# Kernel optimization log

Measured on AMD Instinct MI355X. Metric: run time of the kernel, lower is better.

## Reference

```python
import jax, jax.numpy as jnp
import numpy as np

D_MODEL = 1024
N_HEAD = 16
D_K = D_MODEL // N_HEAD


def setup_inputs() -> dict:
    key = jax.random.key(0)
    ks = jax.random.split(key, 11)
    B, S = 2, 2048
    std = 1.0 / np.sqrt(D_MODEL)
    inp = {
        "Q": jax.random.normal(ks[0], (B, S, D_MODEL), jnp.float32),
        "K": jax.random.normal(ks[1], (B, S, D_MODEL), jnp.float32),
        "V": jax.random.normal(ks[2], (B, S, D_MODEL), jnp.float32),
        "Wq": jax.random.normal(ks[3], (D_MODEL, D_MODEL), jnp.float32) * std,
        "bq": jnp.zeros((D_MODEL,), jnp.float32),
        "Wk": jax.random.normal(ks[4], (D_MODEL, D_MODEL), jnp.float32) * std,
        "bk": jnp.zeros((D_MODEL,), jnp.float32),
        "Wv": jax.random.normal(ks[5], (D_MODEL, D_MODEL), jnp.float32) * std,
        "bv": jnp.zeros((D_MODEL,), jnp.float32),
        "Wo": jax.random.normal(ks[6], (D_MODEL, D_MODEL), jnp.float32) * std,
        "bo": jnp.zeros((D_MODEL,), jnp.float32),
    }
    return inp


def _split_heads(x):
    # [B, S, D] -> [B, H, S, d_k]
    B, S, _ = x.shape
    return x.reshape(B, S, N_HEAD, D_K).transpose(0, 2, 1, 3)


def reference(Q, K, V, Wq, bq, Wk, bk, Wv, bv, Wo, bo):
    q = _split_heads(Q @ Wq.T + bq)   # [B,H,S,dk]
    k = _split_heads(K @ Wk.T + bk)
    v = _split_heads(V @ Wv.T + bv)
    scale = 1.0 / jnp.sqrt(jnp.float32(D_K))
    scores = jnp.einsum("bhqd,bhkd->bhqk", q, k) * scale
    attn = jax.nn.softmax(scores, axis=-1)
    ctx = jnp.einsum("bhqk,bhkd->bhqd", attn, v)  # [B,H,S,dk]
    B, H, S, dk = ctx.shape
    ctx = ctx.transpose(0, 2, 1, 3).reshape(B, S, H * dk)
    return ctx @ Wo.T + bo
```

## Files before the change

### kernel.cpp

```cpp
#include <hip/hip_runtime.h>
#include <hip/hip_bf16.h>
#include <cstdint>
#include <cstddef>
#include <cmath>

typedef __attribute__((ext_vector_type(8))) short short8;
typedef __attribute__((ext_vector_type(4))) short short4_t;
typedef __attribute__((ext_vector_type(4))) float f32x4;
typedef __attribute__((ext_vector_type(16))) float f32x16;

constexpr int B_ = 2, S_ = 2048, H_ = 16, DK_ = 64, DM_ = 1024;

__device__ inline unsigned short f2bf(float x) {
  union { float f; unsigned u; } c; c.f = x;
  unsigned r = c.u + 0x7FFF + ((c.u >> 16) & 1);
  return (unsigned short)(r >> 16);
}

__device__ inline float ex2(float x) {
#if __has_builtin(__builtin_amdgcn_exp2f)
  return __builtin_amdgcn_exp2f(x);
#else
  return exp2f(x);
#endif
}

__device__ inline unsigned pkbf(float lo, float hi) {
  unsigned u;
  asm("v_cvt_pk_bf16_f32 %0, %1, %2" : "=v"(u) : "v"(lo), "v"(hi));
  return u;
}

__device__ inline void plswap(unsigned& a, unsigned& b) {
#if __has_builtin(__builtin_amdgcn_permlane32_swap)
  auto r = __builtin_amdgcn_permlane32_swap(a, b, false, false);
  a = (unsigned)r[0];
  b = (unsigned)r[1];
#else
  unsigned sa = __shfl_xor(a, 32), sb = __shfl_xor(b, 32);
  unsigned lid = __builtin_amdgcn_mbcnt_hi(~0u, __builtin_amdgcn_mbcnt_lo(~0u, 0));
  bool hi = lid >= 32;
  unsigned na = hi ? sb : a;
  unsigned nb = hi ? b : sa;
  a = na; b = nb;
#endif
}

__device__ inline float red_half_sum(float x) {
  unsigned a = __float_as_uint(x), b = a;
  plswap(a, b);
  return __uint_as_float(a) + __uint_as_float(b);
}

__device__ inline f32x4 mfma16(short8 a, short8 b, f32x4 c) {
  return __builtin_amdgcn_mfma_f32_16x16x32_bf16(a, b, c, 0, 0, 0);
}
__device__ inline f32x16 mfma32(short8 a, short8 b, f32x16 c) {
  return __builtin_amdgcn_mfma_f32_32x32x16_bf16(a, b, c, 0, 0, 0);
}

__device__ inline void glds16(const unsigned short* g, unsigned short* l) {
  __builtin_amdgcn_global_load_lds(
      (const __attribute__((address_space(1))) unsigned int*)g,
      (__attribute__((address_space(3))) unsigned int*)l, 16, 0, 0);
}

__global__ __launch_bounds__(256) void cvt_all(
    const float* __restrict__ Q, const float* __restrict__ K,
    const float* __restrict__ V, const float* __restrict__ Wq,
    const float* __restrict__ Wk, const float* __restrict__ Wv,
    const float* __restrict__ Wo, unsigned short* __restrict__ Qb,
    unsigned short* __restrict__ Kb, unsigned short* __restrict__ Vb,
    unsigned short* __restrict__ Wqb, unsigned short* __restrict__ Wkb,
    unsigned short* __restrict__ Wvb, unsigned short* __restrict__ Wob) {
  int bid = blockIdx.x;
  const float* in; unsigned short* out; int off;
  if (bid < 4096)       { in = Q;  out = Qb;  off = bid; }
  else if (bid < 8192)  { in = K;  out = Kb;  off = bid - 4096; }
  else if (bid < 12288) { in = V;  out = Vb;  off = bid - 8192; }
  else if (bid < 13312) { in = Wq; out = Wqb; off = bid - 12288; }
  else if (bid < 14336) { in = Wk; out = Wkb; off = bid - 13312; }
  else if (bid < 15360) { in = Wv; out = Wvb; off = bid - 14336; }
  else                  { in = Wo; out = Wob; off = bid - 15360; }
  int i = off * 256 + threadIdx.x;
  float4 f = ((const float4*)in)[i];
  uint2 o;
  o.x = pkbf(f.x, f.y);
  o.y = pkbf(f.z, f.w);
  ((uint2*)out)[i] = o;
}

__device__ inline void store_out(float* p, float v) { *p = v; }
__device__ inline void store_out(unsigned short* p, float v) { *p = f2bf(v); }

template <typename OUT_T>
__device__ inline void gemm_k3_body(const unsigned short* __restrict__ A,
                                    const unsigned short* __restrict__ Bw,
                                    const float* __restrict__ bias,
                                    OUT_T* __restrict__ C, float cscale,
                                    int bm, int bn) {
  constexpr int Kd = 1024, Nd = 1024, NSTEP = Kd / 64;
  __shared__ unsigned short As[3][128][64];
  __shared__ unsigned short Bs[3][64][64];

  const int tid = threadIdx.x;
  const int lane = tid & 63, wave = tid >> 6;
  const int li = lane & 15, lg = lane >> 4;
  const int wm = wave >> 1, wn = wave & 1;

  const f32x4 zero4 = {0.f, 0.f, 0.f, 0.f};
  f32x4 acc[4][2];
#pragma unroll
  for (int i = 0; i < 4; i++)
#pragma unroll
    for (int j = 0; j < 2; j++) acc[i][j] = zero4;

  const int stg_row = tid >> 3;
  const int ssl = tid & 7;
  const int scol = (ssl ^ (stg_row & 7)) * 8;
  const unsigned short* Ag = A + (size_t)(bm * 128 + stg_row) * Kd + scol;
  const unsigned short* Bg = Bw + (size_t)(bn * 64 + stg_row) * Kd + scol;

  auto stage = [&](int s, int kt) {
    const int kof = kt * 64;
#pragma unroll
    for (int i = 0; i < 4; i++)
      glds16(Ag + (size_t)(i * 32) * Kd + kof,
             &As[s][i * 32 + stg_row][ssl * 8]);
#pragma unroll
    for (int i = 0; i < 2; i++)
      glds16(Bg + (size_t)(i * 32) * Kd + kof,
             &Bs[s][i * 32 + stg_row][ssl * 8]);
  };

  stage(0, 0);
  stage(1, 1);

  const int lswz = li & 7;
  int buf = 0;
  for (int kt = 0; kt < NSTEP; kt++) {
    if (kt < NSTEP - 1)
      asm volatile("s_waitcnt vmcnt(6)" ::: "memory");
    else
      asm volatile("s_waitcnt vmcnt(0)" ::: "memory");
    __builtin_amdgcn_sched_barrier(0);
    __builtin_amdgcn_s_barrier();
    __builtin_amdgcn_sched_barrier(0);

    if (kt + 2 < NSTEP) {
      int nb = buf + 2;
      if (nb >= 3) nb -= 3;
      stage(nb, kt + 2);
    }
    __builtin_amdgcn_sched_barrier(0);

    short8 af[4][2], bf[2][2];
#pragma unroll
    for (int kb = 0; kb < 2; kb++) {
#pragma unroll
      for (int i = 0; i < 4; i++)
        af[i][kb] = *(const short8*)
            &As[buf][wm * 64 + i * 16 + li][((kb * 4 + lg) ^ lswz) * 8];
#pragma unroll
      for (int j = 0; j < 2; j++)
        bf[j][kb] = *(const short8*)
            &Bs[buf][wn * 32 + j * 16 + li][((kb * 4 + lg) ^ lswz) * 8];
    }
#pragma unroll
    for (int kb = 0; kb < 2; kb++)
#pragma unroll
      for (int i = 0; i < 4; i++)
#pragma unroll
        for (int j = 0; j < 2; j++)
          acc[i][j] = mfma16(af[i][kb], bf[j][kb], acc[i][j]);

    buf++;
    if (buf == 3) buf = 0;
  }

#pragma unroll
  for (int j = 0; j < 2; j++) {
    int col = bn * 64 + wn * 32 + j * 16 + li;
    float bv = bias[col];
#pragma unroll
    for (int i = 0; i < 4; i++) {
      int row0 = bm * 128 + wm * 64 + i * 16 + lg * 4;
#pragma unroll
      for (int r = 0; r < 4; r++)
        store_out(&C[(size_t)(row0 + r) * Nd + col], (acc[i][j][r] + bv) * cscale);
    }
  }
}

__global__ __launch_bounds__(256, 2) void gemm_qkv(
    const unsigned short* __restrict__ Aq, const unsigned short* __restrict__ Ak,
    const unsigned short* __restrict__ Av, const unsigned short* __restrict__ Bq,
    const unsigned short* __restrict__ Bk, const unsigned short* __restrict__ Bv,
    const float* __restrict__ bq, const float* __restrict__ bk,
    const float* __restrict__ bv, unsigned short* __restrict__ Cq,
    unsigned short* __restrict__ Ck, unsigned short* __restrict__ Cv,
    float qscale) {
  const int z = blockIdx.z;
  const unsigned short* A = z == 0 ? Aq : z == 1 ? Ak : Av;
  const unsigned short* Bw = z == 0 ? Bq : z == 1 ? Bk : Bv;
  const float* bi = z == 0 ? bq : z == 1 ? bk : bv;
  unsigned short* C = z == 0 ? Cq : z == 1 ? Ck : Cv;
  gemm_k3_body(A, Bw, bi, C, z == 0 ? qscale : 1.0f, blockIdx.x, blockIdx.y);
}

__global__ __launch_bounds__(256, 2) void gemm_out(
    const unsigned short* __restrict__ A, const unsigned short* __restrict__ Bw,
    const float* __restrict__ bias, float* __restrict__ C) {
  gemm_k3_body(A, Bw, bias, C, 1.0f, blockIdx.x, blockIdx.y);
}

struct V4 { short8 v[4]; };

__device__ __forceinline__ void attn_tile_step(
    int kt, int buf, int NT,
    const unsigned short* kg, const unsigned short* vg,
    unsigned short* KsAll, unsigned short* VtAll,
    int srow, int sc, int scs, int key2, int dq,
    const short8* qf, int l31, int h,
    V4& vc, V4& vn, f32x16* po, float& l_lane) {
  unsigned short* KsB = KsAll + buf * (128 * 64);
  unsigned short* VtB = VtAll + buf * (64 * 128);
  unsigned short* KsO = KsAll + (buf ^ 1) * (128 * 64);

  asm volatile("s_waitcnt vmcnt(0)" ::: "memory");
  __builtin_amdgcn_sched_barrier(0);

#pragma unroll
  for (int j = 0; j < 16; j++) {
    const int half = j >> 3, jj = j & 7;
    unsigned w = (unsigned)(unsigned short)vc.v[half][jj] |
                 ((unsigned)(unsigned short)vc.v[2 + half][jj] << 16);
    const int slot = (key2 >> 3) ^ j;
    *(unsigned*)&VtB[(dq * 16 + j) * 128 + slot * 8 + (key2 & 7)] = w;
  }

  if (kt + 1 < NT) {
    const unsigned short* vp =
        vg + (size_t)((kt + 1) * 128 + key2) * DM_ + dq * 16;
    vn.v[0] = *(const short8*)(vp);
    vn.v[1] = *(const short8*)(vp + 8);
    vn.v[2] = *(const short8*)(vp + DM_);
    vn.v[3] = *(const short8*)(vp + DM_ + 8);
  }

  asm volatile("s_waitcnt lgkmcnt(0)" ::: "memory");
  __builtin_amdgcn_sched_barrier(0);
  __builtin_amdgcn_s_barrier();
  __builtin_amdgcn_sched_barrier(0);

  if (kt + 1 < NT) {
    const unsigned short* kgt = kg + (size_t)((kt + 1) * 128) * DM_;
#pragma unroll
    for (int i = 0; i < 4; i++)
      glds16(kgt + (size_t)(i * 32 + srow) * DM_ + scs,
             &KsO[(i * 32 + srow) * 64 + sc * 8]);
  }
  __builtin_amdgcn_sched_barrier(0);

  f32x16 sacc[4];
#pragma unroll
  for (int kb = 0; kb < 4; kb++)
#pragma unroll
    for (int r = 0; r < 16; r++) sacc[kb][r] = 0.f;

  __builtin_amdgcn_s_setprio(1);
#pragma unroll
  for (int tq = 0; tq < 4; tq++) {
    const int sl = ((((tq << 1) | h) ^ (l31 & 7))) * 8;
#pragma unroll
    for (int kb = 0; kb < 4; kb++) {
      short8 kf = *(const short8*)&KsB[(kb * 32 + l31) * 64 + sl];
      sacc[kb] = mfma32(kf, qf[tq], sacc[kb]);
    }
  }
  __builtin_amdgcn_s_setprio(0);

  float s0 = 0.f, s1 = 0.f, s2 = 0.f, s3 = 0.f;
#pragma unroll
  for (int kb = 0; kb < 4; kb++) {
#pragma unroll
    for (int r = 0; r < 16; r += 4) {
      float p0 = ex2(sacc[kb][r]);
      float p1 = ex2(sacc[kb][r + 1]);
      float p2 = ex2(sacc[kb][r + 2]);
      float p3 = ex2(sacc[kb][r + 3]);
      sacc[kb][r] = p0; sacc[kb][r + 1] = p1;
      sacc[kb][r + 2] = p2; sacc[kb][r + 3] = p3;
      s0 += p0; s1 += p1; s2 += p2; s3 += p3;
    }
    unsigned u[4][2];
#pragma unroll
    for (int qd = 0; qd < 4; qd++) {
      u[qd][0] = pkbf(sacc[kb][4 * qd], sacc[kb][4 * qd + 1]);
      u[qd][1] = pkbf(sacc[kb][4 * qd + 2], sacc[kb][4 * qd + 3]);
    }
    __builtin_amdgcn_s_setprio(1);
#pragma unroll
    for (int tt = 0; tt < 2; tt++) {
      const int tp = 2 * kb + tt;
      unsigned x0 = u[2 * tt][0], x1 = u[2 * tt][1];
      unsigned y0 = u[2 * tt + 1][0], y1 = u[2 * tt + 1][1];
      plswap(x0, y0);
      plswap(x1, y1);
      union { unsigned w[4]; short8 v8; } fr;
      fr.w[0] = x0;
      fr.w[1] = x1;
      fr.w[2] = y0;
      fr.w[3] = y1;
      const int slbase = (tp << 1) | h;
#pragma unroll
      for (int db = 0; db < 2; db++) {
        const int row = db * 32 + l31;
        short8 vf = *(const short8*)
            &VtB[row * 128 + (slbase ^ (l31 & 15)) * 8];
        po[db] = mfma32(vf, fr.v8, po[db]);
      }
    }
    __builtin_amdgcn_s_setprio(0);
  }
  l_lane += (s0 + s1) + (s2 + s3);
}

__global__ __launch_bounds__(256, 2) void attn_fwd(
    const unsigned short* __restrict__ q, const unsigned short* __restrict__ k,
    const unsigned short* __restrict__ v, unsigned short* __restrict__ ctx) {
  __shared__ unsigned short Ks[2][128][64];
  __shared__ unsigned short Vt[2][64][128];

  const int tid = threadIdx.x;
  const int lane = tid & 63, wave = tid >> 6;
  const int l31 = lane & 31, h = lane >> 5;
  const int n = blockIdx.x;
  const int xcd = n & 7, m = n >> 3;
  const int bh = xcd * 4 + (m & 3);
  const int qt = m >> 2;
  const int b = bh >> 4, hd = bh & 15;

  const int qrow = qt * 128 + wave * 32 + l31;
  const unsigned short* qg = q + (size_t)(b * S_ + qrow) * DM_ + hd * DK_;
  short8 qf[4];
#pragma unroll
  for (int t = 0; t < 4; t++) qf[t] = *(const short8*)(qg + t * 16 + h * 8);

  f32x16 po[2];
#pragma unroll
  for (int db = 0; db < 2; db++)
#pragma unroll
    for (int r = 0; r < 16; r++) po[db][r] = 0.f;
  float l_lane = 0.f;

  const int srow = tid >> 3, sc = tid & 7;
  const int scs = (sc ^ (srow & 7)) * 8;
  const unsigned short* kg = k + (size_t)(b * S_) * DM_ + hd * DK_;

  const int key2 = (tid & 63) * 2, dq = tid >> 6;
  const unsigned short* vg = v + (size_t)(b * S_) * DM_ + hd * DK_;

  const int NT = S_ / 128;

#pragma unroll
  for (int i = 0; i < 4; i++)
    glds16(kg + (size_t)(i * 32 + srow) * DM_ + scs,
           &Ks[0][i * 32 + srow][sc * 8]);
  V4 va, vb;
  {
    const unsigned short* vp = vg + (size_t)key2 * DM_ + dq * 16;
    va.v[0] = *(const short8*)(vp);
    va.v[1] = *(const short8*)(vp + 8);
    va.v[2] = *(const short8*)(vp + DM_);
    va.v[3] = *(const short8*)(vp + DM_ + 8);
  }

  unsigned short* KsAll = &Ks[0][0][0];
  unsigned short* VtAll = &Vt[0][0][0];
  for (int it = 0; it < NT; it += 2) {
    attn_tile_step(it, 0, NT, kg, vg, KsAll, VtAll, srow, sc, scs, key2, dq,
                   qf, l31, h, va, vb, po, l_lane);
    attn_tile_step(it + 1, 1, NT, kg, vg, KsAll, VtAll, srow, sc, scs, key2,
                   dq, qf, l31, h, vb, va, po, l_lane);
  }

  float l_i = red_half_sum(l_lane);
  float rl = 1.0f / l_i;
  unsigned short* cg = ctx + (size_t)(b * S_ + qrow) * DM_ + hd * DK_;
#pragma unroll
  for (int db = 0; db < 2; db++)
#pragma unroll
    for (int rq = 0; rq < 4; rq++) {
      uint2 w2;
      w2.x = pkbf(po[db][4 * rq] * rl, po[db][4 * rq + 1] * rl);
      w2.y = pkbf(po[db][4 * rq + 2] * rl, po[db][4 * rq + 3] * rl);
      *(uint2*)(cg + db * 32 + 8 * rq + 4 * h) = w2;
    }
}

extern "C" void kernel_launch(void* const* d_in, const int* in_sizes, int n_in,
                              void* d_out, int out_size, void* d_ws, size_t ws_size,
                              hipStream_t stream) {
  const float* Q  = (const float*)d_in[0];
  const float* Kx = (const float*)d_in[1];
  const float* V  = (const float*)d_in[2];
  const float* Wq = (const float*)d_in[3];
  const float* bq = (const float*)d_in[4];
  const float* Wk = (const float*)d_in[5];
  const float* bk = (const float*)d_in[6];
  const float* Wv = (const float*)d_in[7];
  const float* bv = (const float*)d_in[8];
  const float* Wo = (const float*)d_in[9];
  const float* bo = (const float*)d_in[10];
  float* out = (float*)d_out;

  char* ws = (char*)d_ws;
  const size_t MB = 1ull << 20;
  unsigned short* Qb  = (unsigned short*)(ws + 0 * MB);
  unsigned short* Kb  = (unsigned short*)(ws + 8 * MB);
  unsigned short* Vb  = (unsigned short*)(ws + 16 * MB);
  unsigned short* Wqb = (unsigned short*)(ws + 24 * MB);
  unsigned short* Wkb = (unsigned short*)(ws + 26 * MB);
  unsigned short* Wvb = (unsigned short*)(ws + 28 * MB);
  unsigned short* Wob = (unsigned short*)(ws + 30 * MB);
  unsigned short* qp  = (unsigned short*)(ws + 32 * MB);
  unsigned short* kp  = (unsigned short*)(ws + 40 * MB);
  unsigned short* vp  = (unsigned short*)(ws + 48 * MB);
  unsigned short* cx  = (unsigned short*)(ws + 56 * MB);

  cvt_all<<<16384, 256, 0, stream>>>(Q, Kx, V, Wq, Wk, Wv, Wo,
                                     Qb, Kb, Vb, Wqb, Wkb, Wvb, Wob);

  gemm_qkv<<<dim3(32, 16, 3), 256, 0, stream>>>(
      Qb, Kb, Vb, Wqb, Wkb, Wvb, bq, bk, bv, qp, kp, vp, 0.18033688f);

  attn_fwd<<<512, 256, 0, stream>>>(qp, kp, vp, cx);

  gemm_out<<<dim3(32, 16), 256, 0, stream>>>(cx, Wob, bo, out);
}
```

Measured before the change: 125.4 us.

## Load K fragments directly from global into registers instead of LDS staging

Removes the shared-memory K tile and its async global-to-LDS copy. Each wave now loads its own 16 short8 K fragments straight from global memory into registers, prefetching the next tile after the QK MFMAs are issued. This drops the LDS traffic and bank pressure for K, but every wave redundantly fetches the full K tile, which quadruples global/L2 reads for K. It also adds 64 VGPRs of live prefetch state, which may hurt occupancy under launch_bounds(256,2).

```diff
diff --git a/kernel.cpp b/kernel.cpp
--- a/kernel.cpp
+++ b/kernel.cpp
@@ -215,17 +215,15 @@
 }
 
 struct V4 { short8 v[4]; };
+struct K16 { short8 f[4][4]; };
 
 __device__ __forceinline__ void attn_tile_step(
     int kt, int buf, int NT,
-    const unsigned short* kg, const unsigned short* vg,
-    unsigned short* KsAll, unsigned short* VtAll,
-    int srow, int sc, int scs, int key2, int dq,
+    const unsigned short* kl, const unsigned short* vg,
+    unsigned short* VtAll, int key2, int dq,
     const short8* qf, int l31, int h,
-    V4& vc, V4& vn, f32x16* po, float& l_lane) {
-  unsigned short* KsB = KsAll + buf * (128 * 64);
+    V4& vc, V4& vn, K16& kfr, f32x16* po, float& l_lane) {
   unsigned short* VtB = VtAll + buf * (64 * 128);
-  unsigned short* KsO = KsAll + (buf ^ 1) * (128 * 64);
 
   asm volatile("s_waitcnt vmcnt(0)" ::: "memory");
   __builtin_amdgcn_sched_barrier(0);
@@ -253,32 +251,29 @@
   __builtin_amdgcn_s_barrier();
   __builtin_amdgcn_sched_barrier(0);
 
+  f32x16 sacc[4];
+#pragma unroll
+  for (int kb = 0; kb < 4; kb++)
+#pragma unroll
+    for (int r = 0; r < 16; r++) sacc[kb][r] = 0.f;
+
+  __builtin_amdgcn_s_setprio(1);
+#pragma unroll
+  for (int tq = 0; tq < 4; tq++)
+#pragma unroll
+    for (int kb = 0; kb < 4; kb++)
+      sacc[kb] = mfma32(kfr.f[tq][kb], qf[tq], sacc[kb]);
+  __builtin_amdgcn_s_setprio(0);
+
   if (kt + 1 < NT) {
-    const unsigned short* kgt = kg + (size_t)((kt + 1) * 128) * DM_;
-#pragma unroll
-    for (int i = 0; i < 4; i++)
-      glds16(kgt + (size_t)(i * 32 + srow) * DM_ + scs,
-             &KsO[(i * 32 + srow) * 64 + sc * 8]);
-  }
-  __builtin_amdgcn_sched_barrier(0);
-
-  f32x16 sacc[4];
-#pragma unroll
-  for (int kb = 0; kb < 4; kb++)
-#pragma unroll
-    for (int r = 0; r < 16; r++) sacc[kb][r] = 0.f;
-
-  __builtin_amdgcn_s_setprio(1);
-#pragma unroll
-  for (int tq = 0; tq < 4; tq++) {
-    const int sl = ((((tq << 1) | h) ^ (l31 & 7))) * 8;
-#pragma unroll
-    for (int kb = 0; kb < 4; kb++) {
-      short8 kf = *(const short8*)&KsB[(kb * 32 + l31) * 64 + sl];
-      sacc[kb] = mfma32(kf, qf[tq], sacc[kb]);
-    }
-  }
-  __builtin_amdgcn_s_setprio(0);
+    const unsigned short* kp =
+        kl + (size_t)((kt + 1) * 128 + l31) * DM_ + h * 8;
+#pragma unroll
+    for (int tq = 0; tq < 4; tq++)
+#pragma unroll
+      for (int kb = 0; kb < 4; kb++)
+        kfr.f[tq][kb] = *(const short8*)(kp + (size_t)(kb * 32) * DM_ + tq * 16);
+  }
 
   float s0 = 0.f, s1 = 0.f, s2 = 0.f, s3 = 0.f;
 #pragma unroll
@@ -329,7 +324,6 @@
 __global__ __launch_bounds__(256, 2) void attn_fwd(
     const unsigned short* __restrict__ q, const unsigned short* __restrict__ k,
     const unsigned short* __restrict__ v, unsigned short* __restrict__ ctx) {
-  __shared__ unsigned short Ks[2][128][64];
   __shared__ unsigned short Vt[2][64][128];
 
   const int tid = threadIdx.x;
@@ -354,19 +348,21 @@
     for (int r = 0; r < 16; r++) po[db][r] = 0.f;
   float l_lane = 0.f;
 
-  const int srow = tid >> 3, sc = tid & 7;
-  const int scs = (sc ^ (srow & 7)) * 8;
-  const unsigned short* kg = k + (size_t)(b * S_) * DM_ + hd * DK_;
-
+  const unsigned short* kl = k + (size_t)(b * S_) * DM_ + hd * DK_;
   const int key2 = (tid & 63) * 2, dq = tid >> 6;
   const unsigned short* vg = v + (size_t)(b * S_) * DM_ + hd * DK_;
 
   const int NT = S_ / 128;
 
-#pragma unroll
-  for (int i = 0; i < 4; i++)
-    glds16(kg + (size_t)(i * 32 + srow) * DM_ + scs,
-           &Ks[0][i * 32 + srow][sc * 8]);
+  K16 kfr;
+  {
+    const unsigned short* kp = kl + (size_t)l31 * DM_ + h * 8;
+#pragma unroll
+    for (int tq = 0; tq < 4; tq++)
+#pragma unroll
+      for (int kb = 0; kb < 4; kb++)
+        kfr.f[tq][kb] = *(const short8*)(kp + (size_t)(kb * 32) * DM_ + tq * 16);
+  }
   V4 va, vb;
   {
     const unsigned short* vp = vg + (size_t)key2 * DM_ + dq * 16;
@@ -376,13 +372,12 @@
     va.v[3] = *(const short8*)(vp + DM_ + 8);
   }
 
-  unsigned short* KsAll = &Ks[0][0][0];
   unsigned short* VtAll = &Vt[0][0][0];
   for (int it = 0; it < NT; it += 2) {
-    attn_tile_step(it, 0, NT, kg, vg, KsAll, VtAll, srow, sc, scs, key2, dq,
-                   qf, l31, h, va, vb, po, l_lane);
-    attn_tile_step(it + 1, 1, NT, kg, vg, KsAll, VtAll, srow, sc, scs, key2,
-                   dq, qf, l31, h, vb, va, po, l_lane);
+    attn_tile_step(it, 0, NT, kl, vg, VtAll, key2, dq,
+                   qf, l31, h, va, vb, kfr, po, l_lane);
+    attn_tile_step(it + 1, 1, NT, kl, vg, VtAll, key2, dq,
+                   qf, l31, h, vb, va, kfr, po, l_lane);
   }
 
   float l_i = red_half_sum(l_lane);
```

Result: slower. 245.6 us (+95.9%).

## Enlarge projection GEMM tiles to 128x128 with double buffering

Applied to the files above, without the earlier changes.

The QKV and output projection GEMMs move from 128x64 tiles with a three-stage LDS pipeline to 128x128 tiles with a two-stage pipeline. Each wave now computes a 64x64 sub-tile, which doubles the MFMA work per LDS fragment load and halves the number of blocks. The aim is better arithmetic intensity and less global and LDS traffic per output. In exchange the prefetch depth drops to one stage with a full vmcnt(0) wait each step, register pressure rises, and the output GEMM launches only 256 blocks, which may underfill the GPU.

```diff
diff --git a/kernel.cpp b/kernel.cpp
--- a/kernel.cpp
+++ b/kernel.cpp
@@ -94,14 +94,14 @@
 __device__ inline void store_out(unsigned short* p, float v) { *p = f2bf(v); }
 
 template <typename OUT_T>
-__device__ inline void gemm_k3_body(const unsigned short* __restrict__ A,
-                                    const unsigned short* __restrict__ Bw,
-                                    const float* __restrict__ bias,
-                                    OUT_T* __restrict__ C, float cscale,
-                                    int bm, int bn) {
+__device__ inline void gemm128_k2_body(const unsigned short* __restrict__ A,
+                                       const unsigned short* __restrict__ Bw,
+                                       const float* __restrict__ bias,
+                                       OUT_T* __restrict__ C, float cscale,
+                                       int bm, int bn) {
   constexpr int Kd = 1024, Nd = 1024, NSTEP = Kd / 64;
-  __shared__ unsigned short As[3][128][64];
-  __shared__ unsigned short Bs[3][64][64];
+  __shared__ unsigned short As[2][128][64];
+  __shared__ unsigned short Bs[2][128][64];
 
   const int tid = threadIdx.x;
   const int lane = tid & 63, wave = tid >> 6;
@@ -109,78 +109,66 @@
   const int wm = wave >> 1, wn = wave & 1;
 
   const f32x4 zero4 = {0.f, 0.f, 0.f, 0.f};
-  f32x4 acc[4][2];
+  f32x4 acc[4][4];
 #pragma unroll
   for (int i = 0; i < 4; i++)
 #pragma unroll
-    for (int j = 0; j < 2; j++) acc[i][j] = zero4;
+    for (int j = 0; j < 4; j++) acc[i][j] = zero4;
 
   const int stg_row = tid >> 3;
   const int ssl = tid & 7;
   const int scol = (ssl ^ (stg_row & 7)) * 8;
   const unsigned short* Ag = A + (size_t)(bm * 128 + stg_row) * Kd + scol;
-  const unsigned short* Bg = Bw + (size_t)(bn * 64 + stg_row) * Kd + scol;
+  const unsigned short* Bg = Bw + (size_t)(bn * 128 + stg_row) * Kd + scol;
 
   auto stage = [&](int s, int kt) {
     const int kof = kt * 64;
 #pragma unroll
-    for (int i = 0; i < 4; i++)
+    for (int i = 0; i < 4; i++) {
       glds16(Ag + (size_t)(i * 32) * Kd + kof,
              &As[s][i * 32 + stg_row][ssl * 8]);
-#pragma unroll
-    for (int i = 0; i < 2; i++)
       glds16(Bg + (size_t)(i * 32) * Kd + kof,
              &Bs[s][i * 32 + stg_row][ssl * 8]);
+    }
   };
 
   stage(0, 0);
-  stage(1, 1);
 
   const int lswz = li & 7;
   int buf = 0;
   for (int kt = 0; kt < NSTEP; kt++) {
-    if (kt < NSTEP - 1)
-      asm volatile("s_waitcnt vmcnt(6)" ::: "memory");
-    else
-      asm volatile("s_waitcnt vmcnt(0)" ::: "memory");
+    asm volatile("s_waitcnt vmcnt(0)" ::: "memory");
     __builtin_amdgcn_sched_barrier(0);
     __builtin_amdgcn_s_barrier();
     __builtin_amdgcn_sched_barrier(0);
 
-    if (kt + 2 < NSTEP) {
-      int nb = buf + 2;
-      if (nb >= 3) nb -= 3;
-      stage(nb, kt + 2);
-    }
+    if (kt + 1 < NSTEP) stage(buf ^ 1, kt + 1);
     __builtin_amdgcn_sched_barrier(0);
 
-    short8 af[4][2], bf[2][2];
-#pragma unroll
-    for (int kb = 0; kb < 2; kb++) {
-#pragma unroll
-      for (int i = 0; i < 4; i++)
+    short8 af[4][2], bf[4][2];
+#pragma unroll
+    for (int kb = 0; kb < 2; kb++)
+#pragma unroll
+      for (int i = 0; i < 4; i++) {
         af[i][kb] = *(const short8*)
             &As[buf][wm * 64 + i * 16 + li][((kb * 4 + lg) ^ lswz) * 8];
-#pragma unroll
-      for (int j = 0; j < 2; j++)
-        bf[j][kb] = *(const short8*)
-            &Bs[buf][wn * 32 + j * 16 + li][((kb * 4 + lg) ^ lswz) * 8];
-    }
+        bf[i][kb] = *(const short8*)
+            &Bs[buf][wn * 64 + i * 16 + li][((kb * 4 + lg) ^ lswz) * 8];
+      }
 #pragma unroll
     for (int kb = 0; kb < 2; kb++)
 #pragma unroll
       for (int i = 0; i < 4; i++)
 #pragma unroll
-        for (int j = 0; j < 2; j++)
+        for (int j = 0; j < 4; j++)
           acc[i][j] = mfma16(af[i][kb], bf[j][kb], acc[i][j]);
 
-    buf++;
-    if (buf == 3) buf = 0;
-  }
-
-#pragma unroll
-  for (int j = 0; j < 2; j++) {
-    int col = bn * 64 + wn * 32 + j * 16 + li;
+    buf ^= 1;
+  }
+
+#pragma unroll
+  for (int j = 0; j < 4; j++) {
+    int col = bn * 128 + wn * 64 + j * 16 + li;
     float bv = bias[col];
 #pragma unroll
     for (int i = 0; i < 4; i++) {
@@ -205,13 +193,13 @@
   const unsigned short* Bw = z == 0 ? Bq : z == 1 ? Bk : Bv;
   const float* bi = z == 0 ? bq : z == 1 ? bk : bv;
   unsigned short* C = z == 0 ? Cq : z == 1 ? Ck : Cv;
-  gemm_k3_body(A, Bw, bi, C, z == 0 ? qscale : 1.0f, blockIdx.x, blockIdx.y);
+  gemm128_k2_body(A, Bw, bi, C, z == 0 ? qscale : 1.0f, blockIdx.x, blockIdx.y);
 }
 
 __global__ __launch_bounds__(256, 2) void gemm_out(
     const unsigned short* __restrict__ A, const unsigned short* __restrict__ Bw,
     const float* __restrict__ bias, float* __restrict__ C) {
-  gemm_k3_body(A, Bw, bias, C, 1.0f, blockIdx.x, blockIdx.y);
+  gemm128_k2_body(A, Bw, bias, C, 1.0f, blockIdx.x, blockIdx.y);
 }
 
 struct V4 { short8 v[4]; };
@@ -432,10 +420,10 @@
   cvt_all<<<16384, 256, 0, stream>>>(Q, Kx, V, Wq, Wk, Wv, Wo,
                                      Qb, Kb, Vb, Wqb, Wkb, Wvb, Wob);
 
-  gemm_qkv<<<dim3(32, 16, 3), 256, 0, stream>>>(
+  gemm_qkv<<<dim3(32, 8, 3), 256, 0, stream>>>(
       Qb, Kb, Vb, Wqb, Wkb, Wvb, bq, bk, bv, qp, kp, vp, 0.18033688f);
 
   attn_fwd<<<512, 256, 0, stream>>>(qp, kp, vp, cx);
 
-  gemm_out<<<dim3(32, 16), 256, 0, stream>>>(cx, Wob, bo, out);
-}
+  gemm_out<<<dim3(32, 8), 256, 0, stream>>>(cx, Wob, bo, out);
+}
```

Measured after the change: 123.1 us. No clear change (-1.8%).
